# Kernel tuning notes

Hardware: AMD Instinct MI355X
Metric: run time of the kernel (lower is better)

## Reference

```python
import jax, jax.numpy as jnp
import numpy as np

NUM_CLASSES = 80
IMG = 608.0
L_COORD, L_NOOBJ, L_CLS = 5.0, 0.5, 1.0
EPS = 1e-7
ANCHORS = jnp.array([[12,16],[19,36],[40,28],[36,75],[76,55],[72,146],
                     [142,110],[192,243],[459,401]], dtype=jnp.float32).reshape(3, 3, 2)


def _iou(b1, b2):
    # boxes in (cx, cy, w, h); broadcastable shapes [..., 4]
    b1x1 = b1[..., 0] - b1[..., 2] * 0.5; b1y1 = b1[..., 1] - b1[..., 3] * 0.5
    b1x2 = b1[..., 0] + b1[..., 2] * 0.5; b1y2 = b1[..., 1] + b1[..., 3] * 0.5
    b2x1 = b2[..., 0] - b2[..., 2] * 0.5; b2y1 = b2[..., 1] - b2[..., 3] * 0.5
    b2x2 = b2[..., 0] + b2[..., 2] * 0.5; b2y2 = b2[..., 1] + b2[..., 3] * 0.5
    iw = jnp.clip(jnp.minimum(b1x2, b2x2) - jnp.maximum(b1x1, b2x1), 0.0)
    ih = jnp.clip(jnp.minimum(b1y2, b2y2) - jnp.maximum(b1y1, b2y1), 0.0)
    inter = iw * ih
    union = (b1x2 - b1x1) * (b1y2 - b1y1) + (b2x2 - b2x1) * (b2y2 - b2y1) - inter + EPS
    return inter / union


def _scale_loss(pred, anchors, targets):
    # pred: [B, A, H, W, 5+C]; anchors: [A, 2] (pixels); targets: [B, T, 5+C]
    B, A, H, W, _ = pred.shape
    C = pred.shape[-1] - 5
    T = targets.shape[1]

    # ---- decode predictions (decodePredictionsStable) ----
    gy, gx = jnp.meshgrid(jnp.arange(H), jnp.arange(W), indexing='ij')
    grid = jnp.stack([gx, gy], axis=-1).astype(pred.dtype)          # [H, W, 2]
    xy = jax.nn.sigmoid(pred[..., :2])
    wh = jnp.clip(pred[..., 2:4], -10.0, 10.0)
    box_xy = jnp.clip((xy + grid) / jnp.array([W, H], dtype=pred.dtype), 0.0, 1.0)
    box_wh = jnp.clip(jnp.exp(wh) * anchors[None, :, None, None, :] / IMG, 0.0, 1.0)
    pbox = jnp.concatenate([box_xy, box_wh], axis=-1)               # [B,A,H,W,4]
    pconf = jax.nn.sigmoid(pred[..., 4])                            # [B,A,H,W]
    pcls = jax.nn.sigmoid(pred[..., 5:])                            # [B,A,H,W,C]

    # ---- build targets (buildTargetsStable, vectorized scatter) ----
    gtbox = jnp.clip(targets[..., :4], 0.0, 1.0)                    # [B,T,4]
    valid = targets[..., 4] > 0                                     # [B,T]
    gxi = jnp.clip((gtbox[..., 0] * W).astype(jnp.int32), 0, W - 1)
    gyi = jnp.clip((gtbox[..., 1] * H).astype(jnp.int32), 0, H - 1)
    abox = jnp.concatenate([jnp.full((A, 2), 0.5, dtype=pred.dtype), anchors / IMG], axis=-1)
    ious = _iou(abox[None, None, :, :], gtbox[:, :, None, :])       # [B,T,A]
    best = jnp.argmax(ious, axis=-1).astype(jnp.int32)              # first max == torch strict '>' loop
    bidx = jnp.broadcast_to(jnp.arange(B, dtype=jnp.int32)[:, None], (B, T))

    flat = ((bidx * A + best) * H + gyi) * W + gxi                  # [B,T]
    order = jnp.arange(B * T, dtype=jnp.int32).reshape(B, T)
    ncells = B * A * H * W
    winner = jnp.full((ncells,), -1, jnp.int32).at[jnp.where(valid, flat, ncells)].max(order, mode='drop')
    keep = valid & (winner[flat] == order)
    bw = jnp.where(keep, bidx, B)                                   # out-of-range -> dropped

    mask = jnp.zeros((B, A, H, W), pred.dtype).at[bw, best, gyi, gxi].set(1.0, mode='drop')
    tbox = jnp.zeros((B, A, H, W, 4), pred.dtype).at[bw, best, gyi, gxi].set(gtbox, mode='drop')
    tcls = jnp.zeros((B, A, H, W, C), pred.dtype).at[bw, best, gyi, gxi].set(targets[..., 5:5 + C], mode='drop')

    npos = jnp.sum(mask)
    nneg = jnp.asarray(mask.size, pred.dtype) - npos

    # ---- coordinate loss: mean(1 - IoU) over positives ----
    coord = jnp.where(npos > 0, jnp.sum((1.0 - _iou(pbox, tbox)) * mask) / jnp.maximum(npos, 1.0), 0.0)

    # ---- confidence loss: BCE sum/npos + lambdaNoObj * BCE sum/nneg ----
    p = jnp.clip(pconf, 1e-10, 1.0 - 1e-10)
    bce = -(mask * jnp.log(p) + (1.0 - mask) * jnp.log1p(-p))
    conf = jnp.sum(bce * mask) / jnp.maximum(npos, 1.0) \
         + L_NOOBJ * jnp.sum(bce * (1.0 - mask)) / jnp.maximum(nneg, 1.0)

    # ---- class loss: BCE mean over positive rows ----
    pc = jnp.clip(pcls, 1e-10, 1.0 - 1e-10)
    tc = jnp.clip(tcls, 0.0, 1.0)
    bcec = -(tc * jnp.log(pc) + (1.0 - tc) * jnp.log1p(-pc))
    cls = jnp.where(npos > 0, jnp.sum(bcec * mask[..., None]) / jnp.maximum(npos * C, 1.0), 0.0)

    return coord, conf, cls


def setup_inputs() -> dict:
    key = jax.random.key(0)
    k0, k1, k2, k3 = jax.random.split(key, 4)
    B, T, C = 16, 50, NUM_CLASSES
    pred0 = jax.random.normal(k0, (B, 3, 76, 76, 5 + C), dtype=jnp.float32)
    pred1 = jax.random.normal(k1, (B, 3, 38, 38, 5 + C), dtype=jnp.float32)
    pred2 = jax.random.normal(k2, (B, 3, 19, 19, 5 + C), dtype=jnp.float32)
    targets = jax.random.uniform(k3, (B, T, 5 + C), dtype=jnp.float32)
    return {"pred0": pred0, "pred1": pred1, "pred2": pred2, "targets": targets}


def reference(pred0, pred1, pred2, targets):
    coord = jnp.float32(0.0); conf = jnp.float32(0.0); cls = jnp.float32(0.0)
    for s, pred in enumerate((pred0, pred1, pred2)):
        c, cf, cl = _scale_loss(pred, ANCHORS[s], targets)
        coord = coord + c; conf = conf + cf; cls = cls + cl
    total = L_COORD * coord + conf + L_CLS * cls
    return total, coord, conf, cls
```

## Files before the change

kernel.cpp:

```cpp
#include <hip/hip_runtime.h>
#include <math.h>

#define BB   16
#define TT   50
#define BT   (BB*TT)
#define NCLS 80
#define IMGF 608.0f

#define H0 76
#define H1 38
#define H2 19
#define N0 277248
#define N1 69312
#define N2 17328
#define NTOT (N0+N1+N2)

#define CELLS_PER_THREAD 8
#define NOOBJ_BLOCKS ((NTOT + 256*CELLS_PER_THREAD - 1) / (256*CELLS_PER_THREAD))

#define POS_BLOCKS_PER_SCALE 200
#define NPOS_BLOCKS (3*POS_BLOCKS_PER_SCALE)
#define NBLK (NOOBJ_BLOCKS + NPOS_BLOCKS)

__constant__ float c_anchors[3][3][2] = {
    {{12.f,16.f},{19.f,36.f},{40.f,28.f}},
    {{36.f,75.f},{76.f,55.f},{72.f,146.f}},
    {{142.f,110.f},{192.f,243.f},{459.f,401.f}}};
__constant__ int c_H[3] = {H0, H1, H2};

__device__ __forceinline__ float sigmoidf_(float x) { return 1.0f / (1.0f + expf(-x)); }
__device__ __forceinline__ float clipf_(float x, float lo, float hi) {
    return fminf(fmaxf(x, lo), hi);
}

__device__ __forceinline__ float iou4(float ax, float ay, float aw, float ah,
                                      float bx, float by, float bw, float bh) {
    float ax1 = ax - aw * 0.5f, ay1 = ay - ah * 0.5f;
    float ax2 = ax + aw * 0.5f, ay2 = ay + ah * 0.5f;
    float bx1 = bx - bw * 0.5f, by1 = by - bh * 0.5f;
    float bx2 = bx + bw * 0.5f, by2 = by + bh * 0.5f;
    float iw = fmaxf(fminf(ax2, bx2) - fmaxf(ax1, bx1), 0.f);
    float ih = fmaxf(fminf(ay2, by2) - fmaxf(ay1, by1), 0.f);
    float inter = iw * ih;
    float uni = (ax2 - ax1) * (ay2 - ay1) + (bx2 - bx1) * (by2 - by1) - inter + 1e-7f;
    return inter / uni;
}

__device__ __forceinline__ int target_cell(const float* tr, int s, float& cx, float& cy,
                                           float& w, float& h, int& best, int& gxi, int& gyi) {
    float t4 = tr[4];
    if (!(t4 > 0.f)) return -1;
    cx = clipf_(tr[0], 0.f, 1.f);
    cy = clipf_(tr[1], 0.f, 1.f);
    w  = clipf_(tr[2], 0.f, 1.f);
    h  = clipf_(tr[3], 0.f, 1.f);
    best = 0;
    float bi = -1e30f;
    #pragma unroll
    for (int a = 0; a < 3; a++) {
        float aw = c_anchors[s][a][0] / IMGF;
        float ah = c_anchors[s][a][1] / IMGF;
        float v = iou4(0.5f, 0.5f, aw, ah, cx, cy, w, h);
        if (v > bi) { bi = v; best = a; }
    }
    int H = c_H[s];
    gxi = (int)(cx * (float)H); gxi = min(max(gxi, 0), H - 1);
    gyi = (int)(cy * (float)H); gyi = min(max(gyi, 0), H - 1);
    return 0;
}

__global__ __launch_bounds__(256) void k_main(const float* __restrict__ p0,
                                              const float* __restrict__ p1,
                                              const float* __restrict__ p2,
                                              const float* __restrict__ targets,
                                              float* __restrict__ noobj_part,
                                              float* __restrict__ pos_part) {
    int blk = blockIdx.x;
    int lane = threadIdx.x & 63;
    int wv = threadIdx.x >> 6;

    if (blk < NOOBJ_BLOCKS) {
        int base = blk * (256 * CELLS_PER_THREAD) + threadIdx.x;
        float vals[CELLS_PER_THREAD];
        #pragma unroll
        for (int k = 0; k < CELLS_PER_THREAD; k++) {
            int g = base + k * 256;
            const float* pred; int c;
            if (g < N0)            { pred = p0; c = g; }
            else if (g < N0 + N1)  { pred = p1; c = g - N0; }
            else                   { pred = p2; c = g - N0 - N1; }
            vals[k] = (g < NTOT) ? pred[(long long)c * 85 + 4] : 0.f;
        }
        float sum[3] = {0.f, 0.f, 0.f};
        #pragma unroll
        for (int k = 0; k < CELLS_PER_THREAD; k++) {
            int g = base + k * 256;
            if (g < NTOT) {
                float p = clipf_(sigmoidf_(vals[k]), 1e-10f, 1.0f);
                float v = -log1pf(-p);
                if (g < N0)           sum[0] += v;
                else if (g < N0 + N1) sum[1] += v;
                else                  sum[2] += v;
            }
        }
        #pragma unroll
        for (int off = 32; off > 0; off >>= 1) {
            sum[0] += __shfl_xor(sum[0], off, 64);
            sum[1] += __shfl_xor(sum[1], off, 64);
            sum[2] += __shfl_xor(sum[2], off, 64);
        }
        __shared__ float sm[4][3];
        if (lane == 0) { sm[wv][0] = sum[0]; sm[wv][1] = sum[1]; sm[wv][2] = sum[2]; }
        __syncthreads();
        if (threadIdx.x < 3)
            noobj_part[blk * 3 + threadIdx.x] =
                sm[0][threadIdx.x] + sm[1][threadIdx.x] + sm[2][threadIdx.x] + sm[3][threadIdx.x];
    } else {
        int bp = blk - NOOBJ_BLOCKS;
        int s = bp / POS_BLOCKS_PER_SCALE;
        int order = (bp % POS_BLOCKS_PER_SCALE) * 4 + wv;

        float v_coord = 0.f, v_obj = 0.f, v_noadj = 0.f, v_cls = 0.f, v_np = 0.f;

        int b = order / TT, t = order % TT;
        const float* tr = targets + order * 85;
        float cx, cy, w, h; int best, gxi, gyi;
        if (target_cell(tr, s, cx, cy, w, h, best, gxi, gyi) == 0) {
            int H = c_H[s];
            int flat = ((b * 3 + best) * H + gyi) * H + gxi;

            bool lost = false;
            int tp = t + 1 + lane;
            if (tp < TT) {
                const float* tr2 = targets + (b * TT + tp) * 85;
                float cx2, cy2, w2, h2; int best2, gxi2, gyi2;
                if (target_cell(tr2, s, cx2, cy2, w2, h2, best2, gxi2, gyi2) == 0) {
                    int flat2 = ((b * 3 + best2) * H + gyi2) * H + gxi2;
                    lost = (flat2 == flat);
                }
            }
            if (__ballot(lost) == 0ull) {
                const float* pred = (s == 0) ? p0 : (s == 1) ? p1 : p2;
                const float* pc = pred + (long long)flat * 85;

                float px = sigmoidf_(pc[0]);
                float py = sigmoidf_(pc[1]);
                float bx = clipf_((px + (float)gxi) / (float)H, 0.f, 1.f);
                float by = clipf_((py + (float)gyi) / (float)H, 0.f, 1.f);
                float aw = c_anchors[s][best][0], ah = c_anchors[s][best][1];
                float bwv = clipf_(expf(clipf_(pc[2], -10.f, 10.f)) * aw / IMGF, 0.f, 1.f);
                float bhv = clipf_(expf(clipf_(pc[3], -10.f, 10.f)) * ah / IMGF, 0.f, 1.f);
                float iou = iou4(bx, by, bwv, bhv, cx, cy, w, h);

                float p = clipf_(sigmoidf_(pc[4]), 1e-10f, 1.0f);

                float pcv = clipf_(sigmoidf_(pc[5 + lane]), 1e-10f, 1.0f);
                float tc  = clipf_(tr[5 + lane], 0.f, 1.f);
                float cl  = -(tc * logf(pcv) + (1.f - tc) * log1pf(-pcv));
                if (lane < NCLS - 64) {
                    float pcv2 = clipf_(sigmoidf_(pc[5 + 64 + lane]), 1e-10f, 1.0f);
                    float tc2  = clipf_(tr[5 + 64 + lane], 0.f, 1.f);
                    cl += -(tc2 * logf(pcv2) + (1.f - tc2) * log1pf(-pcv2));
                }
                #pragma unroll
                for (int off = 32; off > 0; off >>= 1) cl += __shfl_xor(cl, off, 64);

                v_coord = 1.f - iou;
                v_obj   = -logf(p);
                v_noadj = -log1pf(-p);
                v_cls   = cl;
                v_np    = 1.f;
            }
        }

        __shared__ float psum[4][5];
        if (lane == 0) {
            psum[wv][0] = v_coord; psum[wv][1] = v_obj; psum[wv][2] = v_noadj;
            psum[wv][3] = v_cls;   psum[wv][4] = v_np;
        }
        __syncthreads();
        if (threadIdx.x < 5) {
            pos_part[bp * 5 + threadIdx.x] =
                psum[0][threadIdx.x] + psum[1][threadIdx.x] +
                psum[2][threadIdx.x] + psum[3][threadIdx.x];
        }
    }
}

__global__ __launch_bounds__(256) void k_final(const float* __restrict__ noobj_part,
                                               const float* __restrict__ pos_part,
                                               float* __restrict__ out) {
    float nsum[3] = {0.f, 0.f, 0.f};
    for (int i = threadIdx.x; i < NOOBJ_BLOCKS; i += 256) {
        #pragma unroll
        for (int s = 0; s < 3; s++) nsum[s] += noobj_part[i * 3 + s];
    }
    float ps[3][5] = {};
    for (int i = threadIdx.x; i < NPOS_BLOCKS; i += 256) {
        int s = i / POS_BLOCKS_PER_SCALE;
        #pragma unroll
        for (int q = 0; q < 5; q++) ps[s][q] += pos_part[i * 5 + q];
    }

    __shared__ float red[18][256];
    #pragma unroll
    for (int s = 0; s < 3; s++) {
        red[s][threadIdx.x] = nsum[s];
        #pragma unroll
        for (int q = 0; q < 5; q++) red[3 + s * 5 + q][threadIdx.x] = ps[s][q];
    }
    __syncthreads();
    for (int off = 128; off > 0; off >>= 1) {
        if (threadIdx.x < off) {
            #pragma unroll
            for (int r = 0; r < 18; r++)
                red[r][threadIdx.x] += red[r][threadIdx.x + off];
        }
        __syncthreads();
    }
    if (threadIdx.x == 0) {
        const float ncell[3] = {(float)N0, (float)N1, (float)N2};
        float coord = 0.f, conf = 0.f, cls = 0.f;
        #pragma unroll
        for (int s = 0; s < 3; s++) {
            float noobjTot = red[s][0];
            float co    = red[3 + s * 5 + 0][0];
            float ob    = red[3 + s * 5 + 1][0];
            float noadj = red[3 + s * 5 + 2][0];
            float cl    = red[3 + s * 5 + 3][0];
            float npos  = red[3 + s * 5 + 4][0];
            float nneg = ncell[s] - npos;
            float dn = fmaxf(npos, 1.f);
            conf += ob / dn + 0.5f * (noobjTot - noadj) / fmaxf(nneg, 1.f);
            if (npos > 0.f) {
                coord += co / dn;
                cls   += cl / fmaxf(npos * (float)NCLS, 1.f);
            }
        }
        out[0] = 5.0f * coord + conf + 1.0f * cls;
        out[1] = coord;
        out[2] = conf;
        out[3] = cls;
    }
}

extern "C" void kernel_launch(void* const* d_in, const int* in_sizes, int n_in,
                              void* d_out, int out_size, void* d_ws, size_t ws_size,
                              hipStream_t stream) {
    const float* p0 = (const float*)d_in[0];
    const float* p1 = (const float*)d_in[1];
    const float* p2 = (const float*)d_in[2];
    const float* tg = (const float*)d_in[3];
    float* out = (float*)d_out;

    char* ws = (char*)d_ws;
    float* noobj_part = (float*)ws;
    float* pos_part   = (float*)(ws + 4096);

    k_main<<<NBLK, 256, 0, stream>>>(p0, p1, p2, tg, noobj_part, pos_part);
    k_final<<<1, 256, 0, stream>>>(noobj_part, pos_part, out);
}
```

Measured before the change: 157.4 us.

## Merge positive-target work into noobj blocks via grid-stride wave loop

Removes the separate positive-target blocks and has every wave of the noobj blocks also process positive target items in a grid-stride loop. Each item now writes its own partial to pos_part instead of doing a block-level shared-memory reduction, and the final kernel sums 2400 entries per term instead of 600. The aim is fewer blocks and no extra block-level synchronisation for the positive path. The cost is that the latency-heavy target work now runs inside the streaming blocks, and the final reduction reads more partials.

Result: slower. 173.3 us (+10.1%).

```diff
diff --git a/kernel.cpp b/kernel.cpp
--- a/kernel.cpp
+++ b/kernel.cpp
@@ -16,11 +16,9 @@
 #define NTOT (N0+N1+N2)
 
 #define CELLS_PER_THREAD 8
-#define NOOBJ_BLOCKS ((NTOT + 256*CELLS_PER_THREAD - 1) / (256*CELLS_PER_THREAD))
-
-#define POS_BLOCKS_PER_SCALE 200
-#define NPOS_BLOCKS (3*POS_BLOCKS_PER_SCALE)
-#define NBLK (NOOBJ_BLOCKS + NPOS_BLOCKS)
+#define NBLK ((NTOT + 256*CELLS_PER_THREAD - 1) / (256*CELLS_PER_THREAD))
+#define NWAVE (NBLK * 4)
+#define NPOS  (3 * BT)
 
 __constant__ float c_anchors[3][3][2] = {
     {{12.f,16.f},{19.f,36.f},{40.f,28.f}},
@@ -79,50 +77,50 @@
     int lane = threadIdx.x & 63;
     int wv = threadIdx.x >> 6;
 
-    if (blk < NOOBJ_BLOCKS) {
-        int base = blk * (256 * CELLS_PER_THREAD) + threadIdx.x;
-        float vals[CELLS_PER_THREAD];
-        #pragma unroll
-        for (int k = 0; k < CELLS_PER_THREAD; k++) {
-            int g = base + k * 256;
-            const float* pred; int c;
-            if (g < N0)            { pred = p0; c = g; }
-            else if (g < N0 + N1)  { pred = p1; c = g - N0; }
-            else                   { pred = p2; c = g - N0 - N1; }
-            vals[k] = (g < NTOT) ? pred[(long long)c * 85 + 4] : 0.f;
-        }
-        float sum[3] = {0.f, 0.f, 0.f};
-        #pragma unroll
-        for (int k = 0; k < CELLS_PER_THREAD; k++) {
-            int g = base + k * 256;
-            if (g < NTOT) {
-                float p = clipf_(sigmoidf_(vals[k]), 1e-10f, 1.0f);
-                float v = -log1pf(-p);
-                if (g < N0)           sum[0] += v;
-                else if (g < N0 + N1) sum[1] += v;
-                else                  sum[2] += v;
-            }
-        }
-        #pragma unroll
-        for (int off = 32; off > 0; off >>= 1) {
-            sum[0] += __shfl_xor(sum[0], off, 64);
-            sum[1] += __shfl_xor(sum[1], off, 64);
-            sum[2] += __shfl_xor(sum[2], off, 64);
-        }
-        __shared__ float sm[4][3];
-        if (lane == 0) { sm[wv][0] = sum[0]; sm[wv][1] = sum[1]; sm[wv][2] = sum[2]; }
-        __syncthreads();
-        if (threadIdx.x < 3)
-            noobj_part[blk * 3 + threadIdx.x] =
-                sm[0][threadIdx.x] + sm[1][threadIdx.x] + sm[2][threadIdx.x] + sm[3][threadIdx.x];
-    } else {
-        int bp = blk - NOOBJ_BLOCKS;
-        int s = bp / POS_BLOCKS_PER_SCALE;
-        int order = (bp % POS_BLOCKS_PER_SCALE) * 4 + wv;
+    int base = blk * (256 * CELLS_PER_THREAD) + threadIdx.x;
+    float vals[CELLS_PER_THREAD];
+    #pragma unroll
+    for (int k = 0; k < CELLS_PER_THREAD; k++) {
+        int g = base + k * 256;
+        const float* pred; int c;
+        if (g < N0)            { pred = p0; c = g; }
+        else if (g < N0 + N1)  { pred = p1; c = g - N0; }
+        else                   { pred = p2; c = g - N0 - N1; }
+        vals[k] = (g < NTOT) ? pred[(long long)c * 85 + 4] : 0.f;
+    }
+    float sum[3] = {0.f, 0.f, 0.f};
+    #pragma unroll
+    for (int k = 0; k < CELLS_PER_THREAD; k++) {
+        int g = base + k * 256;
+        if (g < NTOT) {
+            float p = clipf_(sigmoidf_(vals[k]), 1e-10f, 1.0f);
+            float v = -log1pf(-p);
+            if (g < N0)           sum[0] += v;
+            else if (g < N0 + N1) sum[1] += v;
+            else                  sum[2] += v;
+        }
+    }
+    #pragma unroll
+    for (int off = 32; off > 0; off >>= 1) {
+        sum[0] += __shfl_xor(sum[0], off, 64);
+        sum[1] += __shfl_xor(sum[1], off, 64);
+        sum[2] += __shfl_xor(sum[2], off, 64);
+    }
+    __shared__ float sm[4][3];
+    if (lane == 0) { sm[wv][0] = sum[0]; sm[wv][1] = sum[1]; sm[wv][2] = sum[2]; }
+    __syncthreads();
+    if (threadIdx.x < 3)
+        noobj_part[blk * 3 + threadIdx.x] =
+            sm[0][threadIdx.x] + sm[1][threadIdx.x] + sm[2][threadIdx.x] + sm[3][threadIdx.x];
+
+    int gw = blk * 4 + wv;
+    for (int item = gw; item < NPOS; item += NWAVE) {
+        int s = item / BT;
+        int order = item % BT;
+        int b = order / TT, t = order % TT;
 
         float v_coord = 0.f, v_obj = 0.f, v_noadj = 0.f, v_cls = 0.f, v_np = 0.f;
 
-        int b = order / TT, t = order % TT;
         const float* tr = targets + order * 85;
         float cx, cy, w, h; int best, gxi, gyi;
         if (target_cell(tr, s, cx, cy, w, h, best, gxi, gyi) == 0) {
@@ -173,16 +171,10 @@
             }
         }
 
-        __shared__ float psum[4][5];
         if (lane == 0) {
-            psum[wv][0] = v_coord; psum[wv][1] = v_obj; psum[wv][2] = v_noadj;
-            psum[wv][3] = v_cls;   psum[wv][4] = v_np;
-        }
-        __syncthreads();
-        if (threadIdx.x < 5) {
-            pos_part[bp * 5 + threadIdx.x] =
-                psum[0][threadIdx.x] + psum[1][threadIdx.x] +
-                psum[2][threadIdx.x] + psum[3][threadIdx.x];
+            float* dst = pos_part + (long long)item * 5;
+            dst[0] = v_coord; dst[1] = v_obj; dst[2] = v_noadj;
+            dst[3] = v_cls;   dst[4] = v_np;
         }
     }
 }
@@ -191,13 +183,13 @@
                                                const float* __restrict__ pos_part,
                                                float* __restrict__ out) {
     float nsum[3] = {0.f, 0.f, 0.f};
-    for (int i = threadIdx.x; i < NOOBJ_BLOCKS; i += 256) {
+    for (int i = threadIdx.x; i < NBLK; i += 256) {
         #pragma unroll
         for (int s = 0; s < 3; s++) nsum[s] += noobj_part[i * 3 + s];
     }
     float ps[3][5] = {};
-    for (int i = threadIdx.x; i < NPOS_BLOCKS; i += 256) {
-        int s = i / POS_BLOCKS_PER_SCALE;
+    for (int i = threadIdx.x; i < NPOS; i += 256) {
+        int s = i / BT;
         #pragma unroll
         for (int q = 0; q < 5; q++) ps[s][q] += pos_part[i * 5 + q];
     }
```
